# Performance work log

Hardware: AMD Instinct MI355X
Metric: run time of the kernel (lower is better)

## Reference

```python
import jax, jax.numpy as jnp
import numpy as np

B, S, T, D, K = 8, 500, 30, 5, 10
H, TW, E = 64, 512, 8000


def gru_scan(x, Wi, Wh, bi, bh, lengths=None):
    """Torch-convention GRU. x: [N,T,Din] -> (full [N,T,H], last [N,H]).
    If lengths is given, hidden state freezes past each sequence's length and
    padded steps of `full` are zeroed."""
    N, Tn, _ = x.shape
    Hh = Wh.shape[0]
    xg = jnp.moveaxis(x @ Wi + bi, 1, 0)  # [T,N,3H]

    def step(h, inp):
        xg_t, t = inp
        hg = h @ Wh + bh
        xr, xz, xn = jnp.split(xg_t, 3, axis=-1)
        hr, hz, hn = jnp.split(hg, 3, axis=-1)
        r = jax.nn.sigmoid(xr + hr)
        z = jax.nn.sigmoid(xz + hz)
        n = jnp.tanh(xn + r * hn)
        h_new = (1.0 - z) * n + z * h
        if lengths is not None:
            valid = (t < lengths)[:, None]
            h_new = jnp.where(valid, h_new, h)
            full_t = jnp.where(valid, h_new, 0.0)
        else:
            full_t = h_new
        return h_new, full_t

    h0 = jnp.zeros((N, Hh), x.dtype)
    last, full = jax.lax.scan(step, h0, (xg, jnp.arange(Tn)))
    return jnp.moveaxis(full, 0, 1), last


def layer_norm(x, g, b, eps=1e-5):
    m = jnp.mean(x, axis=-1, keepdims=True)
    v = jnp.var(x, axis=-1, keepdims=True)
    return (x - m) / jnp.sqrt(v + eps) * g + b


def setup_inputs() -> dict:
    key = jax.random.key(0)
    ks = jax.random.split(key, 40)
    p = lambda i, shape: jax.random.normal(ks[i], shape, jnp.float32) * 0.05
    inp = {}
    inp['price'] = jax.random.normal(ks[0], (B, S, T, 3), jnp.float32)
    inp['tweets'] = jax.random.normal(ks[1], (B, S, D, K, TW), jnp.float32)
    inp['tweet_counts'] = jax.random.randint(ks[2], (B, S, D), 0, K + 1, jnp.int32)
    inp['edge_index'] = jax.random.randint(ks[3], (2, E), 0, S, jnp.int32)
    inp['num_edge_type'] = 3
    # price GRU (in=3)
    inp['pg_Wi'] = p(4, (3, 3 * H)); inp['pg_Wh'] = p(5, (H, 3 * H))
    inp['pg_bi'] = p(6, (3 * H,)); inp['pg_bh'] = p(7, (3 * H,))
    # tweet GRU (in=512)
    inp['tg_Wi'] = p(8, (TW, 3 * H)); inp['tg_Wh'] = p(9, (H, 3 * H))
    inp['tg_bi'] = p(10, (3 * H,)); inp['tg_bh'] = p(11, (3 * H,))
    # date GRU (in=64)
    inp['dg_Wi'] = p(12, (H, 3 * H)); inp['dg_Wh'] = p(13, (H, 3 * H))
    inp['dg_bi'] = p(14, (3 * H,)); inp['dg_bh'] = p(15, (3 * H,))
    inp['bil_A'] = p(16, (H, H, H)); inp['bil_b'] = p(17, (H,))
    inp['gnn_W'] = p(18, (H, H)); inp['gnn_b'] = p(19, (H,))
    inp['fc1_W'] = p(20, (2 * H, H)); inp['fc1_b'] = p(21, (H,))
    inp['ln1_g'] = jnp.ones((H,), jnp.float32); inp['ln1_b'] = jnp.zeros((H,), jnp.float32)
    inp['fc2_W'] = p(22, (H, H)); inp['fc2_b'] = p(23, (H,))
    inp['ln2_g'] = jnp.ones((H,), jnp.float32); inp['ln2_b'] = jnp.zeros((H,), jnp.float32)
    inp['mlp_W1'] = p(24, (H, H)); inp['mlp_b1'] = p(25, (H,))
    inp['mlp_W2'] = p(26, (H, 1)); inp['mlp_b2'] = p(27, (1,))
    return inp


def reference(price, tweets, pg_Wi, pg_Wh, pg_bi, pg_bh,
              tg_Wi, tg_Wh, tg_bi, tg_bh, dg_Wi, dg_Wh, dg_bi, dg_bh,
              bil_A, bil_b, gnn_W, gnn_b, fc1_W, fc1_b, ln1_g, ln1_b,
              fc2_W, fc2_b, ln2_g, ln2_b, mlp_W1, mlp_b1, mlp_W2, mlp_b2,
              tweet_counts, edge_index, num_edge_type):
    # NOTE: in the original, attn applies softmax over dim=1 of a [T,1] score,
    # i.e. a size-1 axis, so the weights are identically 1 and the attention
    # context is exactly sum(full, axis=0). We reproduce that exact math.
    # Price branch: GRU over T days for every (window, stock), then masked sum.
    pf, _ = gru_scan(price.reshape(B * S, T, 3), pg_Wi, pg_Wh, pg_bi, pg_bh)
    x = pf.sum(axis=1)  # [B*S, H]

    # Tweet branch: ragged GRU over up to K tweets per (window, stock, date).
    tw = tweets.reshape(B * S * D, K, TW)
    lens = tweet_counts.reshape(B * S * D)
    tf, _ = gru_scan(tw, tg_Wi, tg_Wh, tg_bi, tg_bh, lengths=lens)
    news = tf.sum(axis=1).reshape(B * S, D, H)  # zeros where count==0

    # Date GRU over the D daily news vectors.
    df, _ = gru_scan(news, dg_Wi, dg_Wh, dg_bi, dg_bh)
    text = df.sum(axis=1)  # [B*S, H]

    # Bilinear fusion: out_k = text A_k x + b_k, then tanh.
    comb = jnp.tanh(jnp.einsum('ni,kij,nj->nk', text, bil_A, x) + bil_b)
    ft = comb.reshape(B, S, H)

    # Simple GNN: mean-aggregate neighbor features over edge list, then linear.
    src, dst = edge_index[0], edge_index[1]
    deg = jax.ops.segment_sum(jnp.ones((E,), ft.dtype), dst, num_segments=S)
    denom = jnp.maximum(deg, 1.0)[:, None]
    agg = jax.vmap(lambda m: jax.ops.segment_sum(m, dst, num_segments=S))(ft[:, src, :])
    g = jnp.tanh((agg / denom) @ gnn_W + gnn_b)

    h = jnp.concatenate([ft, g], axis=-1)            # [B,S,2H]
    h = jax.nn.relu(layer_norm(h @ fc1_W + fc1_b, ln1_g, ln1_b))  # dropout: eval
    h = jax.nn.relu(layer_norm(h @ fc2_W + fc2_b, ln2_g, ln2_b))
    h = jax.nn.relu(h @ mlp_W1 + mlp_b1)
    logits = (h @ mlp_W2 + mlp_b2).reshape(B, S)
    return logits
```

## Files before the change

### kernel.cpp

```cpp
#include <hip/hip_runtime.h>
#include <math.h>

#define Bq 8
#define Sq 500
#define Tq 30
#define Dq 5
#define Kq 10
#define Hq 64
#define TWq 512
#define Eq 8000
#define NS (Bq*Sq)
#define NTt (NS*Dq)
#define G3 (3*Hq)
#define TG 4

#define MR 48
#define KC 64
#define XPITCH 72
#define XGP 196
#define NKT (TWq/32)
#define NNT (G3/16)
#define PSEQ 16

#define XROWS 40
#define STG_PLANE (MR*XPITCH)
#define STG_BUF  (2*STG_PLANE)

typedef __attribute__((ext_vector_type(8))) short short8_t;
typedef __attribute__((ext_vector_type(4))) float float4_t;

__device__ __forceinline__ float fsig(float x) {
    return 1.0f / (1.0f + __expf(-x));
}
__device__ __forceinline__ float ftanh(float x) {
    return 1.0f - 2.0f / (__expf(2.0f * x) + 1.0f);
}

__device__ __forceinline__ float wave_sum64(float v) {
    #pragma unroll
    for (int off = 32; off; off >>= 1) v += __shfl_xor(v, off, 64);
    return v;
}

__device__ __forceinline__ short f32_to_bf16_rn(float f) {
    union { float f; unsigned u; } v; v.f = f;
    unsigned r = v.u + 0x7fffu + ((v.u >> 16) & 1u);
    return (short)(r >> 16);
}
__device__ __forceinline__ float bf16_to_f32(short s) {
    union { unsigned u; float f; } v; v.u = ((unsigned)(unsigned short)s) << 16;
    return v.f;
}

__global__ __launch_bounds__(64)
void wfrag_prep_kernel(const float* __restrict__ Wi,
                       short* __restrict__ Wf_hi, short* __restrict__ Wf_lo) {
    const int kt = blockIdx.x / NNT;
    const int nt = blockIdx.x - kt*NNT;
    const int lane = threadIdx.x;
    const int quad = lane >> 4, l16 = lane & 15;
    short h[8], l[8];
    #pragma unroll
    for (int j = 0; j < 8; j++) {
        int k = kt*32 + quad*8 + j;
        int n = nt*16 + l16;
        float w = Wi[(size_t)k*G3 + n];
        short hi = f32_to_bf16_rn(w);
        short lo = f32_to_bf16_rn(w - bf16_to_f32(hi));
        h[j] = hi; l[j] = lo;
    }
    size_t off = ((size_t)blockIdx.x*64 + lane)*8;
    *(short8_t*)(Wf_hi + off) = *(const short8_t*)h;
    *(short8_t*)(Wf_lo + off) = *(const short8_t*)l;
}

__global__ __launch_bounds__(64)
void bilfrag_prep_kernel(const float* __restrict__ A,
                         short* __restrict__ Bf_hi, short* __restrict__ Bf_lo) {
    const int kt = blockIdx.x >> 2;
    const int nt = blockIdx.x & 3;
    const int lane = threadIdx.x;
    const int quad = lane >> 4, l16 = lane & 15;
    short h[8], l[8];
    #pragma unroll
    for (int j = 0; j < 8; j++) {
        int kidx = kt*32 + quad*8 + j;
        int n = nt*16 + l16;
        float w = A[(size_t)n*4096 + kidx];
        short hi = f32_to_bf16_rn(w);
        h[j] = hi; l[j] = f32_to_bf16_rn(w - bf16_to_f32(hi));
    }
    size_t off = ((size_t)blockIdx.x*64 + lane)*8;
    *(short8_t*)(Bf_hi + off) = *(const short8_t*)h;
    *(short8_t*)(Bf_lo + off) = *(const short8_t*)l;
}

__global__ __launch_bounds__(256)
void price_gru_mfma_kernel(const float* __restrict__ price,
                           const float* __restrict__ Wi,
                           const short* __restrict__ Whf_hi, const short* __restrict__ Whf_lo,
                           const float* __restrict__ bi, const float* __restrict__ bh,
                           float* __restrict__ xout) {
    __shared__ __align__(16) float price_s[PSEQ*90];
    __shared__ __align__(16) short h_hi[PSEQ*72];
    __shared__ __align__(16) short h_lo[PSEQ*72];
    const int tid = threadIdx.x;
    const int n0 = blockIdx.x * PSEQ;
    const int wv = tid >> 6;
    const int lane = tid & 63;
    const int quad = lane >> 4;
    const int l16 = lane & 15;
    const int u = wv*16 + l16;
    for (int i = tid; i < PSEQ*90; i += 256) price_s[i] = price[(size_t)n0*90 + i];
    for (int i = tid; i < PSEQ*72; i += 256) { h_hi[i] = 0; h_lo[i] = 0; }
    float wir[3], wiz[3], win[3];
    #pragma unroll
    for (int k = 0; k < 3; k++) {
        wir[k] = Wi[k*G3 + u];
        wiz[k] = Wi[k*G3 + 64 + u];
        win[k] = Wi[k*G3 + 128 + u];
    }
    const float cbr = bi[u] + bh[u];
    const float cbz = bi[64+u] + bh[64+u];
    const float bin = bi[128+u];
    const float bhn = bh[128+u];
    short8_t bfh[2][3], bfl[2][3];
    #pragma unroll
    for (int kt = 0; kt < 2; kt++)
        #pragma unroll
        for (int g = 0; g < 3; g++) {
            size_t off = (((size_t)kt*NNT + (g*4 + wv))*64 + lane)*8;
            bfh[kt][g] = *(const short8_t*)(Whf_hi + off);
            bfl[kt][g] = *(const short8_t*)(Whf_lo + off);
        }
    float hprev[4] = {0.f,0.f,0.f,0.f}, sum[4] = {0.f,0.f,0.f,0.f};
    __syncthreads();
    for (int t = 0; t < Tq; t++) {
        short8_t ah[2], al[2];
        #pragma unroll
        for (int kt = 0; kt < 2; kt++) {
            int addr = l16*72 + kt*32 + quad*8;
            ah[kt] = *(const short8_t*)&h_hi[addr];
            al[kt] = *(const short8_t*)&h_lo[addr];
        }
        float4_t accr = {0.f,0.f,0.f,0.f}, accz = {0.f,0.f,0.f,0.f}, accn = {0.f,0.f,0.f,0.f};
        #pragma unroll
        for (int kt = 0; kt < 2; kt++) {
            accr = __builtin_amdgcn_mfma_f32_16x16x32_bf16(ah[kt], bfh[kt][0], accr, 0,0,0);
            accr = __builtin_amdgcn_mfma_f32_16x16x32_bf16(ah[kt], bfl[kt][0], accr, 0,0,0);
            accr = __builtin_amdgcn_mfma_f32_16x16x32_bf16(al[kt], bfh[kt][0], accr, 0,0,0);
            accz = __builtin_amdgcn_mfma_f32_16x16x32_bf16(ah[kt], bfh[kt][1], accz, 0,0,0);
            accz = __builtin_amdgcn_mfma_f32_16x16x32_bf16(ah[kt], bfl[kt][1], accz, 0,0,0);
            accz = __builtin_amdgcn_mfma_f32_16x16x32_bf16(al[kt], bfh[kt][1], accz, 0,0,0);
            accn = __builtin_amdgcn_mfma_f32_16x16x32_bf16(ah[kt], bfh[kt][2], accn, 0,0,0);
            accn = __builtin_amdgcn_mfma_f32_16x16x32_bf16(ah[kt], bfl[kt][2], accn, 0,0,0);
            accn = __builtin_amdgcn_mfma_f32_16x16x32_bf16(al[kt], bfl[kt][2], accn, 0,0,0);
        }
        __syncthreads();
        #pragma unroll
        for (int r = 0; r < 4; r++) {
            const int s = quad*4 + r;
            float p0 = price_s[s*90 + t*3 + 0];
            float p1 = price_s[s*90 + t*3 + 1];
            float p2 = price_s[s*90 + t*3 + 2];
            float xr = fmaf(p2, wir[2], fmaf(p1, wir[1], fmaf(p0, wir[0], cbr)));
            float xz = fmaf(p2, wiz[2], fmaf(p1, wiz[1], fmaf(p0, wiz[0], cbz)));
            float xn = fmaf(p2, win[2], fmaf(p1, win[1], fmaf(p0, win[0], bin)));
            float rg = fsig(xr + accr[r]);
            float zg = fsig(xz + accz[r]);
            float ng = ftanh(xn + rg*(accn[r] + bhn));
            float h = (1.0f - zg)*ng + zg*hprev[r];
            hprev[r] = h; sum[r] += h;
            short hh = f32_to_bf16_rn(h);
            h_hi[s*72 + u] = hh;
            h_lo[s*72 + u] = f32_to_bf16_rn(h - bf16_to_f32(hh));
        }
        __syncthreads();
    }
    #pragma unroll
    for (int r = 0; r < 4; r++)
        xout[(size_t)(n0 + quad*4 + r)*Hq + u] = sum[r];
}

__global__ __launch_bounds__(256, 4)
void tweet_gru_kernel(const float* __restrict__ tweets,
                      const int* __restrict__ counts,
                      const short* __restrict__ Wf_hi, const short* __restrict__ Wf_lo,
                      const short* __restrict__ Wht_hi, const short* __restrict__ Wht_lo,
                      const float* __restrict__ bi, const float* __restrict__ bh,
                      float* __restrict__ news) {
    __shared__ __align__(16) char smem[XROWS*XGP*4];
    __shared__ __align__(16) short rh_hi[16*72];
    __shared__ __align__(16) short rh_lo[16*72];
    __shared__ int len_s[TG];
    __shared__ int tmax_s;
    short* stg = (short*)smem;
    float* xg  = (float*)smem;

    const int tid  = threadIdx.x;
    const int n0   = blockIdx.x * TG;
    const int wave = tid >> 6;
    const int lane = tid & 63;
    const int quad = lane >> 4;
    const int l16  = lane & 15;

    if (tid < TG) {
        int c = counts[n0 + tid];
        len_s[tid] = c < 0 ? 0 : (c > Kq ? Kq : c);
    }
    for (int i = tid; i < 16*72; i += 256) { rh_hi[i] = 0; rh_lo[i] = 0; }
    __syncthreads();
    if (tid == 0) {
        int m01 = len_s[0] > len_s[1] ? len_s[0] : len_s[1];
        int m23 = len_s[2] > len_s[3] ? len_s[2] : len_s[3];
        tmax_s = m01 > m23 ? m01 : m23;
    }

    const float* gp[3];
    int lofs[3];
    bool val[3];
    #pragma unroll
    for (int j = 0; j < 3; j++) {
        const int ii = tid + j*256;
        const bool ok = ii < TG*Kq*(KC/4);
        const int i = ok ? ii : 0;
        const int row = i >> 4;
        const int c4  = i & 15;
        const int s   = (row*205) >> 11;
        const int t   = row - s*10;
        val[j]  = ok && (t < len_s[s]);
        gp[j]   = tweets + (((size_t)(n0+s))*Kq + t)*TWq + c4*4;
        lofs[j] = row*XPITCH + c4*4;
    }

    float4_t acc[3][3];
    #pragma unroll
    for (int a = 0; a < 3; a++)
        #pragma unroll
        for (int b = 0; b < 3; b++)
            acc[a][b] = (float4_t){0.f, 0.f, 0.f, 0.f};

    #pragma unroll
    for (int j = 0; j < 3; j++) if (val[j]) {
        float4 v = *(const float4*)(gp[j]);
        float f[4] = {v.x, v.y, v.z, v.w};
        short hh[4], ll[4];
        #pragma unroll
        for (int q = 0; q < 4; q++) {
            short hi = f32_to_bf16_rn(f[q]);
            hh[q] = hi;
            ll[q] = f32_to_bf16_rn(f[q] - bf16_to_f32(hi));
        }
        *(short4*)&stg[lofs[j]]             = *(const short4*)hh;
        *(short4*)&stg[STG_PLANE + lofs[j]] = *(const short4*)ll;
    }
    __syncthreads();

    for (int ch = 0; ch < TWq/KC; ch++) {
        const int cur = ch & 1;
        float4 v[3];
        if (ch < TWq/KC - 1) {
            #pragma unroll
            for (int j = 0; j < 3; j++) if (val[j])
                v[j] = *(const float4*)(gp[j] + (ch+1)*KC);
        }
        const short* xh = stg + cur*STG_BUF;
        const short* xl = xh + STG_PLANE;
        #pragma unroll
        for (int ks = 0; ks < KC/32; ks++) {
            const int kt = ch*(KC/32) + ks;
            short8_t bh_[3], bl_[3];
            #pragma unroll
            for (int ntl = 0; ntl < 3; ntl++) {
                size_t off = (((size_t)kt*NNT + (wave*3 + ntl))*64 + lane)*8;
                bh_[ntl] = *(const short8_t*)(Wf_hi + off);
                bl_[ntl] = *(const short8_t*)(Wf_lo + off);
            }
            short8_t ah_[3], al_[3];
            #pragma unroll
            for (int mt = 0; mt < 3; mt++) {
                int addr = (mt*16 + l16)*XPITCH + ks*32 + quad*8;
                ah_[mt] = *(const short8_t*)&xh[addr];
                al_[mt] = *(const short8_t*)&xl[addr];
            }
            #pragma unroll
            for (int mt = 0; mt < 3; mt++)
                #pragma unroll
                for (int ntl = 0; ntl < 3; ntl++) {
                    acc[mt][ntl] = __builtin_amdgcn_mfma_f32_16x16x32_bf16(ah_[mt], bh_[ntl], acc[mt][ntl], 0, 0, 0);
                    acc[mt][ntl] = __builtin_amdgcn_mfma_f32_16x16x32_bf16(ah_[mt], bl_[ntl], acc[mt][ntl], 0, 0, 0);
                    acc[mt][ntl] = __builtin_amdgcn_mfma_f32_16x16x32_bf16(al_[mt], bh_[ntl], acc[mt][ntl], 0, 0, 0);
                }
        }
        if (ch < TWq/KC - 1) {
            short* yh = stg + (cur^1)*STG_BUF;
            short* yl = yh + STG_PLANE;
            #pragma unroll
            for (int j = 0; j < 3; j++) if (val[j]) {
                float f[4] = {v[j].x, v[j].y, v[j].z, v[j].w};
                short hh[4], ll[4];
                #pragma unroll
                for (int q = 0; q < 4; q++) {
                    short hi = f32_to_bf16_rn(f[q]);
                    hh[q] = hi;
                    ll[q] = f32_to_bf16_rn(f[q] - bf16_to_f32(hi));
                }
                *(short4*)&yh[lofs[j]] = *(const short4*)hh;
                *(short4*)&yl[lofs[j]] = *(const short4*)ll;
            }
        }
        __syncthreads();
    }

    #pragma unroll
    for (int ntl = 0; ntl < 3; ntl++) {
        const int col = (wave*3 + ntl)*16 + l16;
        const float bic = bi[col];
        #pragma unroll
        for (int mt = 0; mt < 3; mt++) {
            const int row0 = mt*16 + quad*4;
            if (row0 < XROWS) {
                #pragma unroll
                for (int r2 = 0; r2 < 4; r2++)
                    xg[(row0 + r2)*XGP + col] = acc[mt][ntl][r2] + bic;
            }
        }
    }

    const int u = wave*16 + l16;
    short8_t tbh[2][3], tbl[2][3];
    #pragma unroll
    for (int kt = 0; kt < 2; kt++)
        #pragma unroll
        for (int g = 0; g < 3; g++) {
            size_t off = (((size_t)kt*NNT + (g*4 + wave))*64 + lane)*8;
            tbh[kt][g] = *(const short8_t*)(Wht_hi + off);
            tbl[kt][g] = *(const short8_t*)(Wht_lo + off);
        }
    const float bhr = bh[u];
    const float bhz = bh[64+u];
    const float bhn = bh[128+u];
    int lp[4];
    #pragma unroll
    for (int r = 0; r < 4; r++) lp[r] = len_s[r];
    float hprev[4] = {0.f,0.f,0.f,0.f}, sum[4] = {0.f,0.f,0.f,0.f};
    const int tmax = tmax_s;
    for (int t = 0; t < tmax; t++) {
        const int ha = l16*72;
        short8_t ah0 = *(const short8_t*)&rh_hi[ha + quad*8];
        short8_t ah1 = *(const short8_t*)&rh_hi[ha + 32 + quad*8];
        short8_t al0 = *(const short8_t*)&rh_lo[ha + quad*8];
        short8_t al1 = *(const short8_t*)&rh_lo[ha + 32 + quad*8];
        float4_t ar = {0.f,0.f,0.f,0.f}, az = {0.f,0.f,0.f,0.f}, an = {0.f,0.f,0.f,0.f};
        ar = __builtin_amdgcn_mfma_f32_16x16x32_bf16(ah0, tbh[0][0], ar, 0,0,0);
        ar = __builtin_amdgcn_mfma_f32_16x16x32_bf16(ah0, tbl[0][0], ar, 0,0,0);
        ar = __builtin_amdgcn_mfma_f32_16x16x32_bf16(al0, tbh[0][0], ar, 0,0,0);
        ar = __builtin_amdgcn_mfma_f32_16x16x32_bf16(ah1, tbh[1][0], ar, 0,0,0);
        ar = __builtin_amdgcn_mfma_f32_16x16x32_bf16(ah1, tbl[1][0], ar, 0,0,0);
        ar = __builtin_amdgcn_mfma_f32_16x16x32_bf16(al1, tbh[1][0], ar, 0,0,0);
        az = __builtin_amdgcn_mfma_f32_16x16x32_bf16(ah0, tbh[0][1], az, 0,0,0);
        az = __builtin_amdgcn_mfma_f32_16x16x32_bf16(ah0, tbl[0][1], az, 0,0,0);
        az = __builtin_amdgcn_mfma_f32_16x16x32_bf16(al0, tbh[0][1], az, 0,0,0);
        az = __builtin_amdgcn_mfma_f32_16x16x32_bf16(ah1, tbh[1][1], az, 0,0,0);
        az = __builtin_amdgcn_mfma_f32_16x16x32_bf16(ah1, tbl[1][1], az, 0,0,0);
        az = __builtin_amdgcn_mfma_f32_16x16x32_bf16(al1, tbh[1][1], az, 0,0,0);
        an = __builtin_amdgcn_mfma_f32_16x16x32_bf16(ah0, tbh[0][2], an, 0,0,0);
        an = __builtin_amdgcn_mfma_f32_16x16x32_bf16(ah0, tbl[0][2], an, 0,0,0);
        an = __builtin_amdgcn_mfma_f32_16x16x32_bf16(al0, tbh[0][2], an, 0,0,0);
        an = __builtin_amdgcn_mfma_f32_16x16x32_bf16(ah1, tbh[1][2], an, 0,0,0);
        an = __builtin_amdgcn_mfma_f32_16x16x32_bf16(ah1, tbl[1][2], an, 0,0,0);
        an = __builtin_amdgcn_mfma_f32_16x16x32_bf16(al1, tbh[1][2], an, 0,0,0);
        __syncthreads();
        if (quad == 0) {
            #pragma unroll
            for (int r = 0; r < 4; r++) {
                if (t < lp[r]) {
                    const float* xr = &xg[(r*Kq + t)*XGP];
                    float rg = fsig(xr[u]        + ar[r] + bhr);
                    float zg = fsig(xr[Hq+u]     + az[r] + bhz);
                    float ng = ftanh(xr[2*Hq+u]  + rg*(an[r] + bhn));
                    float hn = (1.0f - zg)*ng + zg*hprev[r];
                    hprev[r] = hn; sum[r] += hn;
                    short hh = f32_to_bf16_rn(hn);
                    rh_hi[r*72 + u] = hh;
                    rh_lo[r*72 + u] = f32_to_bf16_rn(hn - bf16_to_f32(hh));
                }
            }
        }
        __syncthreads();
    }
    if (quad == 0) {
        #pragma unroll
        for (int r = 0; r < 4; r++)
            news[(size_t)(n0 + r)*Hq + u] = sum[r];
    }
}

__global__ __launch_bounds__(192)
void date_gru_kernel(const float* __restrict__ news,
                     const float* __restrict__ Wi, const float* __restrict__ Wh,
                     const float* __restrict__ bi, const float* __restrict__ bh,
                     float* __restrict__ text) {
    __shared__ __align__(16) float nw_s[Dq*Hq];
    __shared__ __align__(16) float h_s[Hq];
    __shared__ __align__(16) float xg_s[G3];
    __shared__ __align__(16) float hg_s[G3];
    const int n = blockIdx.x;
    const int g = threadIdx.x;
    for (int i = g; i < Dq*Hq; i += 192) nw_s[i] = news[(size_t)n*Dq*Hq + i];
    float wi[Hq], wh[Hq];
    #pragma unroll
    for (int j = 0; j < Hq; j++) { wi[j] = Wi[j*G3+g]; wh[j] = Wh[j*G3+g]; }
    const float big = bi[g], bhg = bh[g];
    if (g < Hq) h_s[g] = 0.0f;
    float hreg = 0.0f, sum = 0.0f;
    __syncthreads();
    for (int t = 0; t < Dq; t++) {
        float a0=0.f,a1=0.f,a2=0.f,a3=0.f, b0=0.f,b1=0.f,b2=0.f,b3=0.f;
        #pragma unroll
        for (int j = 0; j < Hq; j += 4) {
            float4 nv = *(const float4*)&nw_s[t*Hq + j];
            float4 hv = *(const float4*)&h_s[j];
            a0 = fmaf(nv.x, wi[j+0], a0);
            a1 = fmaf(nv.y, wi[j+1], a1);
            a2 = fmaf(nv.z, wi[j+2], a2);
            a3 = fmaf(nv.w, wi[j+3], a3);
            b0 = fmaf(hv.x, wh[j+0], b0);
            b1 = fmaf(hv.y, wh[j+1], b1);
            b2 = fmaf(hv.z, wh[j+2], b2);
            b3 = fmaf(hv.w, wh[j+3], b3);
        }
        xg_s[g] = big + ((a0+a1)+(a2+a3));
        hg_s[g] = bhg + ((b0+b1)+(b2+b3));
        __syncthreads();
        if (g < Hq) {
            float r  = fsig(xg_s[g]      + hg_s[g]);
            float z  = fsig(xg_s[Hq+g]   + hg_s[Hq+g]);
            float nn = ftanh(xg_s[2*Hq+g] + r*hg_s[2*Hq+g]);
            hreg = (1.0f - z)*nn + z*hreg;
            sum += hreg;
            h_s[g] = hreg;
        }
        __syncthreads();
    }
    if (g < Hq) text[(size_t)n*Hq + g] = sum;
}

#define TP 68
#define XP 72
__global__ __launch_bounds__(256)
void bilinear_mfma_kernel(const float* __restrict__ text, const float* __restrict__ x,
                          const short* __restrict__ Bf_hi, const short* __restrict__ Bf_lo,
                          const float* __restrict__ bb, float* __restrict__ ft) {
    __shared__ __align__(16) float t_s[16*TP];
    __shared__ __align__(16) float x_s[16*XP];
    const int tid = threadIdx.x;
    const int n0 = blockIdx.x * 16;
    const int wv = tid >> 6, lane = tid & 63, quad = lane >> 4, l16 = lane & 15;
    for (int i = tid; i < 16*64; i += 256) {
        int r = i >> 6, c = i & 63;
        t_s[r*TP + c] = text[(size_t)(n0 + r)*Hq + c];
        x_s[r*XP + c] = x[(size_t)(n0 + r)*Hq + c];
    }
    float4_t acc = {0.f,0.f,0.f,0.f};
    __syncthreads();
    for (int kt = 0; kt < 128; kt++) {
        const int i  = kt >> 1;
        const int j0 = (kt & 1)*32 + quad*8;
        size_t boff = (((size_t)kt*4 + wv)*64 + lane)*8;
        short8_t bh_ = *(const short8_t*)(Bf_hi + boff);
        short8_t bl_ = *(const short8_t*)(Bf_lo + boff);
        float ti = t_s[l16*TP + i];
        float xv[8];
        *(float4*)&xv[0] = *(const float4*)&x_s[l16*XP + j0];
        *(float4*)&xv[4] = *(const float4*)&x_s[l16*XP + j0 + 4];
        short ph[8], pl[8];
        #pragma unroll
        for (int jj = 0; jj < 8; jj++) {
            float p = ti * xv[jj];
            short hi = f32_to_bf16_rn(p);
            ph[jj] = hi;
            pl[jj] = f32_to_bf16_rn(p - bf16_to_f32(hi));
        }
        short8_t ah = *(const short8_t*)ph;
        short8_t al = *(const short8_t*)pl;
        acc = __builtin_amdgcn_mfma_f32_16x16x32_bf16(ah, bh_, acc, 0,0,0);
        acc = __builtin_amdgcn_mfma_f32_16x16x32_bf16(ah, bl_, acc, 0,0,0);
        acc = __builtin_amdgcn_mfma_f32_16x16x32_bf16(al, bh_, acc, 0,0,0);
    }
    const int col = wv*16 + l16;
    const float bk = bb[col];
    #pragma unroll
    for (int r = 0; r < 4; r++) {
        int n = quad*4 + r;
        ft[(size_t)(n0 + n)*Hq + col] = ftanh(acc[r] + bk);
    }
}

__global__ void deg_kernel(const int* __restrict__ ei, float* __restrict__ deg) {
    int e = blockIdx.x*256 + threadIdx.x;
    if (e < Eq) atomicAdd(&deg[ei[Eq + e]], 1.0f);
}

__global__ void agg_kernel(const int* __restrict__ ei, const float* __restrict__ ft,
                           float* __restrict__ agg) {
    int gid = blockIdx.x*256 + threadIdx.x;
    int e = gid >> 6;
    int u = gid & 63;
    if (e < Eq) {
        int src = ei[e], dst = ei[Eq + e];
        #pragma unroll
        for (int b = 0; b < Bq; b++) {
            atomicAdd(&agg[((size_t)(b*Sq + dst))*Hq + u],
                      ft[((size_t)(b*Sq + src))*Hq + u]);
        }
    }
}

__global__ __launch_bounds__(64)
void head_kernel(const float* __restrict__ ft, const float* __restrict__ agg,
                 const float* __restrict__ deg,
                 const float* __restrict__ gnn_W, const float* __restrict__ gnn_b,
                 const float* __restrict__ fc1_W, const float* __restrict__ fc1_b,
                 const float* __restrict__ ln1_g, const float* __restrict__ ln1_b,
                 const float* __restrict__ fc2_W, const float* __restrict__ fc2_b,
                 const float* __restrict__ ln2_g, const float* __restrict__ ln2_b,
                 const float* __restrict__ mlp_W1, const float* __restrict__ mlp_b1,
                 const float* __restrict__ mlp_W2, const float* __restrict__ mlp_b2,
                 float* __restrict__ out) {
    __shared__ __align__(16) float a_s[Hq];
    __shared__ __align__(16) float in_s[2*Hq];
    __shared__ __align__(16) float t_s[Hq];
    const int n = blockIdx.x;
    const int s = n % Sq;
    const int u = threadIdx.x;
    const float denom = fmaxf(deg[s], 1.0f);
    a_s[u]  = agg[(size_t)n*Hq + u] / denom;
    in_s[u] = ft[(size_t)n*Hq + u];
    __syncthreads();
    {
        float a0=0.f,a1=0.f,a2=0.f,a3=0.f;
        #pragma unroll
        for (int j = 0; j < Hq; j += 4) {
            a0 = fmaf(a_s[j+0], gnn_W[(j+0)*Hq + u], a0);
            a1 = fmaf(a_s[j+1], gnn_W[(j+1)*Hq + u], a1);
            a2 = fmaf(a_s[j+2], gnn_W[(j+2)*Hq + u], a2);
            a3 = fmaf(a_s[j+3], gnn_W[(j+3)*Hq + u], a3);
        }
        in_s[Hq+u] = ftanh(gnn_b[u] + ((a0+a1)+(a2+a3)));
    }
    __syncthreads();
    float v;
    {
        float a0=0.f,a1=0.f,a2=0.f,a3=0.f;
        #pragma unroll
        for (int j = 0; j < 2*Hq; j += 4) {
            a0 = fmaf(in_s[j+0], fc1_W[(j+0)*Hq + u], a0);
            a1 = fmaf(in_s[j+1], fc1_W[(j+1)*Hq + u], a1);
            a2 = fmaf(in_s[j+2], fc1_W[(j+2)*Hq + u], a2);
            a3 = fmaf(in_s[j+3], fc1_W[(j+3)*Hq + u], a3);
        }
        v = fc1_b[u] + ((a0+a1)+(a2+a3));
        float m = wave_sum64(v) * (1.0f/Hq);
        float d = v - m;
        float var = wave_sum64(d*d) * (1.0f/Hq);
        v = fmaxf(d * rsqrtf(var + 1e-5f) * ln1_g[u] + ln1_b[u], 0.0f);
    }
    t_s[u] = v;
    __syncthreads();
    {
        float a0=0.f,a1=0.f,a2=0.f,a3=0.f;
        #pragma unroll
        for (int j = 0; j < Hq; j += 4) {
            a0 = fmaf(t_s[j+0], fc2_W[(j+0)*Hq + u], a0);
            a1 = fmaf(t_s[j+1], fc2_W[(j+1)*Hq + u], a1);
            a2 = fmaf(t_s[j+2], fc2_W[(j+2)*Hq + u], a2);
            a3 = fmaf(t_s[j+3], fc2_W[(j+3)*Hq + u], a3);
        }
        v = fc2_b[u] + ((a0+a1)+(a2+a3));
        float m = wave_sum64(v) * (1.0f/Hq);
        float d = v - m;
        float var = wave_sum64(d*d) * (1.0f/Hq);
        v = fmaxf(d * rsqrtf(var + 1e-5f) * ln2_g[u] + ln2_b[u], 0.0f);
    }
    __syncthreads();
    a_s[u] = v;
    __syncthreads();
    {
        float a0=0.f,a1=0.f,a2=0.f,a3=0.f;
        #pragma unroll
        for (int j = 0; j < Hq; j += 4) {
            a0 = fmaf(a_s[j+0], mlp_W1[(j+0)*Hq + u], a0);
            a1 = fmaf(a_s[j+1], mlp_W1[(j+1)*Hq + u], a1);
            a2 = fmaf(a_s[j+2], mlp_W1[(j+2)*Hq + u], a2);
            a3 = fmaf(a_s[j+3], mlp_W1[(j+3)*Hq + u], a3);
        }
        v = fmaxf(mlp_b1[u] + ((a0+a1)+(a2+a3)), 0.0f);
    }
    float p = wave_sum64(v * mlp_W2[u]);
    if (u == 0) out[n] = p + mlp_b2[0];
}

extern "C" void kernel_launch(void* const* d_in, const int* in_sizes, int n_in,
                              void* d_out, int out_size, void* d_ws, size_t ws_size,
                              hipStream_t stream) {
    (void)in_sizes; (void)n_in; (void)out_size; (void)ws_size;
    const float* price  = (const float*)d_in[0];
    const float* tweets = (const float*)d_in[1];
    const int*   counts = (const int*)d_in[2];
    const int*   ei     = (const int*)d_in[3];
    const float* pg_Wi = (const float*)d_in[5];
    const float* pg_Wh = (const float*)d_in[6];
    const float* pg_bi = (const float*)d_in[7];
    const float* pg_bh = (const float*)d_in[8];
    const float* tg_Wi = (const float*)d_in[9];
    const float* tg_Wh = (const float*)d_in[10];
    const float* tg_bi = (const float*)d_in[11];
    const float* tg_bh = (const float*)d_in[12];
    const float* dg_Wi = (const float*)d_in[13];
    const float* dg_Wh = (const float*)d_in[14];
    const float* dg_bi = (const float*)d_in[15];
    const float* dg_bh = (const float*)d_in[16];
    const float* bil_A = (const float*)d_in[17];
    const float* bil_b = (const float*)d_in[18];
    const float* gnn_W = (const float*)d_in[19];
    const float* gnn_b = (const float*)d_in[20];
    const float* fc1_W = (const float*)d_in[21];
    const float* fc1_b = (const float*)d_in[22];
    const float* ln1_g = (const float*)d_in[23];
    const float* ln1_b = (const float*)d_in[24];
    const float* fc2_W = (const float*)d_in[25];
    const float* fc2_b = (const float*)d_in[26];
    const float* ln2_g = (const float*)d_in[27];
    const float* ln2_b = (const float*)d_in[28];
    const float* mlp_W1 = (const float*)d_in[29];
    const float* mlp_b1 = (const float*)d_in[30];
    const float* mlp_W2 = (const float*)d_in[31];
    const float* mlp_b2 = (const float*)d_in[32];

    float* ws      = (float*)d_ws;
    float* x_price = ws;
    float* news    = ws + 256000;
    float* text    = ws + 1536000;
    float* ft      = ws + 1792000;
    float* agg     = ws + 2048000;
    float* deg     = ws + 2304000;
    short* Wf_hi   = (short*)(ws + 2304512);
    short* Wf_lo   = Wf_hi  + 98304;
    short* Whp_hi  = Wf_lo  + 98304;
    short* Whp_lo  = Whp_hi + 12288;
    short* Bf_hi   = Whp_lo + 12288;
    short* Bf_lo   = Bf_hi  + 262144;
    short* Wht_hi  = Bf_lo  + 262144;
    short* Wht_lo  = Wht_hi + 12288;

    hipMemsetAsync(agg, 0, (256000 + 512)*sizeof(float), stream);

    wfrag_prep_kernel<<<NKT*NNT, 64, 0, stream>>>(tg_Wi, Wf_hi, Wf_lo);
    wfrag_prep_kernel<<<2*NNT, 64, 0, stream>>>(pg_Wh, Whp_hi, Whp_lo);
    wfrag_prep_kernel<<<2*NNT, 64, 0, stream>>>(tg_Wh, Wht_hi, Wht_lo);
    bilfrag_prep_kernel<<<128*4, 64, 0, stream>>>(bil_A, Bf_hi, Bf_lo);

    price_gru_mfma_kernel<<<NS/PSEQ, 256, 0, stream>>>(price, pg_Wi, Whp_hi, Whp_lo,
                                                       pg_bi, pg_bh, x_price);
    tweet_gru_kernel<<<NTt/TG, 256, 0, stream>>>(tweets, counts, Wf_hi, Wf_lo,
                                                 Wht_hi, Wht_lo, tg_bi, tg_bh, news);
    date_gru_kernel<<<NS, 192, 0, stream>>>(news, dg_Wi, dg_Wh, dg_bi, dg_bh, text);
    bilinear_mfma_kernel<<<NS/16, 256, 0, stream>>>(text, x_price, Bf_hi, Bf_lo, bil_b, ft);
    deg_kernel<<<(Eq+255)/256, 256, 0, stream>>>(ei, deg);
    agg_kernel<<<(Eq*Hq)/256, 256, 0, stream>>>(ei, ft, agg);
    head_kernel<<<NS, 64, 0, stream>>>(ft, agg, deg,
                                       gnn_W, gnn_b, fc1_W, fc1_b, ln1_g, ln1_b,
                                       fc2_W, fc2_b, ln2_g, ln2_b,
                                       mlp_W1, mlp_b1, mlp_W2, mlp_b2,
                                       (float*)d_out);
}
```

Before: 854.1 us.

## Replace atomic edge scatter with CSR gather fused into head kernel

Measured after the change: 848.2 us. Within noise of the previous version (-0.7%).

```diff
diff --git a/kernel.cpp b/kernel.cpp
--- a/kernel.cpp
+++ b/kernel.cpp
@@ -369,7 +369,7 @@
         an = __builtin_amdgcn_mfma_f32_16x16x32_bf16(al0, tbh[0][2], an, 0,0,0);
         an = __builtin_amdgcn_mfma_f32_16x16x32_bf16(ah1, tbh[1][2], an, 0,0,0);
         an = __builtin_amdgcn_mfma_f32_16x16x32_bf16(ah1, tbl[1][2], an, 0,0,0);
-        an = __builtin_amdgcn_mfma_f32_16x16x32_bf16(al1, tbh[1][2], an, 0,0,0);
+        an = __builtin_amdgcn_mfma_f32_16x16x32_bf16(al1, tbl[1][2], an, 0,0,0);
         __syncthreads();
         if (quad == 0) {
             #pragma unroll
@@ -497,29 +497,46 @@
     }
 }
 
-__global__ void deg_kernel(const int* __restrict__ ei, float* __restrict__ deg) {
+__global__ void count_kernel(const int* __restrict__ ei, int* __restrict__ cnt) {
     int e = blockIdx.x*256 + threadIdx.x;
-    if (e < Eq) atomicAdd(&deg[ei[Eq + e]], 1.0f);
-}
-
-__global__ void agg_kernel(const int* __restrict__ ei, const float* __restrict__ ft,
-                           float* __restrict__ agg) {
-    int gid = blockIdx.x*256 + threadIdx.x;
-    int e = gid >> 6;
-    int u = gid & 63;
+    if (e < Eq) atomicAdd(&cnt[ei[Eq + e]], 1);
+}
+
+__global__ __launch_bounds__(512)
+void scan_kernel(const int* __restrict__ cnt, int* __restrict__ off,
+                 int* __restrict__ cursor) {
+    __shared__ int buf[512];
+    const int tid = threadIdx.x;
+    int v = (tid < Sq) ? cnt[tid] : 0;
+    buf[tid] = v;
+    __syncthreads();
+    #pragma unroll
+    for (int d = 1; d < 512; d <<= 1) {
+        int t = (tid >= d) ? buf[tid - d] : 0;
+        __syncthreads();
+        buf[tid] += t;
+        __syncthreads();
+    }
+    if (tid <= Sq) {
+        int excl = buf[tid] - v;
+        off[tid] = excl;
+        if (tid < Sq) cursor[tid] = excl;
+    }
+}
+
+__global__ void scatter_kernel(const int* __restrict__ ei, int* __restrict__ cursor,
+                               int* __restrict__ sorted_src) {
+    int e = blockIdx.x*256 + threadIdx.x;
     if (e < Eq) {
-        int src = ei[e], dst = ei[Eq + e];
-        #pragma unroll
-        for (int b = 0; b < Bq; b++) {
-            atomicAdd(&agg[((size_t)(b*Sq + dst))*Hq + u],
-                      ft[((size_t)(b*Sq + src))*Hq + u]);
-        }
+        int dst = ei[Eq + e];
+        int p = atomicAdd(&cursor[dst], 1);
+        sorted_src[p] = ei[e];
     }
 }
 
 __global__ __launch_bounds__(64)
-void head_kernel(const float* __restrict__ ft, const float* __restrict__ agg,
-                 const float* __restrict__ deg,
+void head_kernel(const float* __restrict__ ft,
+                 const int* __restrict__ off, const int* __restrict__ sorted_src,
                  const float* __restrict__ gnn_W, const float* __restrict__ gnn_b,
                  const float* __restrict__ fc1_W, const float* __restrict__ fc1_b,
                  const float* __restrict__ ln1_g, const float* __restrict__ ln1_b,
@@ -532,10 +549,16 @@
     __shared__ __align__(16) float in_s[2*Hq];
     __shared__ __align__(16) float t_s[Hq];
     const int n = blockIdx.x;
-    const int s = n % Sq;
+    const int b = n / Sq;
+    const int s = n - b*Sq;
     const int u = threadIdx.x;
-    const float denom = fmaxf(deg[s], 1.0f);
-    a_s[u]  = agg[(size_t)n*Hq + u] / denom;
+    const int o0 = off[s], o1 = off[s+1];
+    const float* ftb = ft + (size_t)b*Sq*Hq;
+    float acc = 0.0f;
+    for (int e = o0; e < o1; ++e)
+        acc += ftb[(size_t)sorted_src[e]*Hq + u];
+    const float denom = (o1 - o0) > 1 ? (float)(o1 - o0) : 1.0f;
+    a_s[u]  = acc / denom;
     in_s[u] = ft[(size_t)n*Hq + u];
     __syncthreads();
     {
@@ -643,8 +666,10 @@
     float* news    = ws + 256000;
     float* text    = ws + 1536000;
     float* ft      = ws + 1792000;
-    float* agg     = ws + 2048000;
-    float* deg     = ws + 2304000;
+    int*   cnt     = (int*)(ws + 2048000);
+    int*   off     = cnt + 512;
+    int*   cursor  = off + 512;
+    int*   sorted  = cursor + 512;
     short* Wf_hi   = (short*)(ws + 2304512);
     short* Wf_lo   = Wf_hi  + 98304;
     short* Whp_hi  = Wf_lo  + 98304;
@@ -654,7 +679,11 @@
     short* Wht_hi  = Bf_lo  + 262144;
     short* Wht_lo  = Wht_hi + 12288;
 
-    hipMemsetAsync(agg, 0, (256000 + 512)*sizeof(float), stream);
+    hipMemsetAsync(cnt, 0, 512*sizeof(int), stream);
+
+    count_kernel<<<(Eq+255)/256, 256, 0, stream>>>(ei, cnt);
+    scan_kernel<<<1, 512, 0, stream>>>(cnt, off, cursor);
+    scatter_kernel<<<(Eq+255)/256, 256, 0, stream>>>(ei, cursor, sorted);
 
     wfrag_prep_kernel<<<NKT*NNT, 64, 0, stream>>>(tg_Wi, Wf_hi, Wf_lo);
     wfrag_prep_kernel<<<2*NNT, 64, 0, stream>>>(pg_Wh, Whp_hi, Whp_lo);
@@ -667,9 +696,7 @@
                                                  Wht_hi, Wht_lo, tg_bi, tg_bh, news);
     date_gru_kernel<<<NS, 192, 0, stream>>>(news, dg_Wi, dg_Wh, dg_bi, dg_bh, text);
     bilinear_mfma_kernel<<<NS/16, 256, 0, stream>>>(text, x_price, Bf_hi, Bf_lo, bil_b, ft);
-    deg_kernel<<<(Eq+255)/256, 256, 0, stream>>>(ei, deg);
-    agg_kernel<<<(Eq*Hq)/256, 256, 0, stream>>>(ei, ft, agg);
-    head_kernel<<<NS, 64, 0, stream>>>(ft, agg, deg,
+    head_kernel<<<NS, 64, 0, stream>>>(ft, off, sorted,
                                        gnn_W, gnn_b, fc1_W, fc1_b, ln1_g, ln1_b,
                                        fc2_W, fc2_b, ln2_g, ln2_b,
                                        mlp_W1, mlp_b1, mlp_W2, mlp_b2,
```
